# Optimization experiments

Hardware: AMD Instinct MI355X
Metric: run time of the kernel (lower is better)

## Reference

```python
import jax, jax.numpy as jnp
import numpy as np

D_MODEL = 1024
NUM_HEADS = 16
D_K = D_MODEL // NUM_HEADS
SCALE = D_K ** -0.5
NEG = -1e9


def _split_heads(t):
    B, L, D = t.shape
    return t.reshape(B, L, NUM_HEADS, D_K).transpose(0, 2, 1, 3)  # (B,H,L,dk)


def _tropical_scores(Q, K):
    # max over d_k of Q[...,i,d] + K[...,j,d] without materializing (B,H,L,L,dk)
    Qd = jnp.moveaxis(Q, -1, 0)  # (dk,B,H,L)
    Kd = jnp.moveaxis(K, -1, 0)
    B, H, L, _ = Q.shape
    init = jnp.full((B, H, L, L), -jnp.inf, Q.dtype)
    def step(carry, qk):
        q, k = qk  # (B,H,L) each
        return jnp.maximum(carry, q[..., :, None] + k[..., None, :]), None
    out, _ = jax.lax.scan(step, init, (Qd, Kd))
    return out


def setup_inputs() -> dict:
    key = jax.random.key(0)
    ks = jax.random.split(key, 10)
    B, L = 2, 1024
    x = jax.random.normal(ks[0], (B, L, D_MODEL), dtype=jnp.float32)
    # causal mask (B,1,L,L)
    mask = jnp.broadcast_to(jnp.tril(jnp.ones((L, L), dtype=bool)), (B, 1, L, L))
    s = 0.02
    Wq = jax.random.normal(ks[1], (D_MODEL, D_MODEL), jnp.float32) * s
    Wk = jax.random.normal(ks[2], (D_MODEL, D_MODEL), jnp.float32) * s
    Wv = jax.random.normal(ks[3], (D_MODEL, D_MODEL), jnp.float32) * s
    Wo = jax.random.normal(ks[4], (D_MODEL, D_MODEL), jnp.float32) * s
    bq = jnp.zeros((D_MODEL,), jnp.float32)
    bk = jnp.zeros((D_MODEL,), jnp.float32)
    bv = jnp.zeros((D_MODEL,), jnp.float32)
    bo = jnp.zeros((D_MODEL,), jnp.float32)
    # score_gate: weight zero-init, bias = -2.0 (as in torch module)
    Wg = jnp.zeros((NUM_HEADS, D_MODEL), jnp.float32)
    bg = jnp.full((NUM_HEADS,), -2.0, jnp.float32)
    # log temperatures, init_temp=1.0 -> log(1)=0
    log_temps = jnp.zeros((NUM_HEADS,), jnp.float32)
    return {"x": x, "mask": mask, "Wq": Wq, "bq": bq, "Wk": Wk, "bk": bk,
            "Wv": Wv, "bv": bv, "Wo": Wo, "bo": bo, "Wg": Wg, "bg": bg,
            "log_temps": log_temps}


def reference(x, mask, Wq, bq, Wk, bk, Wv, bv, Wo, bo, Wg, bg, log_temps):
    B, L, D = x.shape
    Q = _split_heads(x @ Wq.T + bq)
    K = _split_heads(x @ Wk.T + bk)
    V = _split_heads(x @ Wv.T + bv)
    class_scores = jnp.einsum('bhqd,bhkd->bhqk', Q, K) * SCALE
    trop_scores = _tropical_scores(Q, K) * SCALE
    # per-query, per-head gate g in (0,1): (B,L,H) -> (B,H,L,1)
    g = jax.nn.sigmoid(x @ Wg.T + bg).transpose(0, 2, 1)[..., None]
    scores = g * trop_scores + (1.0 - g) * class_scores
    scores = jnp.where(mask, scores, NEG)
    tau = jnp.clip(jnp.exp(log_temps), 0.02, 10.0).reshape(1, NUM_HEADS, 1, 1)
    attn = jax.nn.softmax(scores / tau, axis=-1)
    out = jnp.einsum('bhqk,bhkd->bhqd', attn, V)
    out = out.transpose(0, 2, 1, 3).reshape(B, L, D)
    return out @ Wo.T + bo, attn
```

## Files before the change

kernel.cpp:

```cpp
#include <hip/hip_runtime.h>


typedef _Float16 f16;
typedef __attribute__((ext_vector_type(2))) _Float16 h2;
typedef __attribute__((ext_vector_type(8))) _Float16 f16x8;
typedef __attribute__((ext_vector_type(4))) float f32x4;

__device__ inline f32x4 mfma_f16(f16x8 a, f16x8 b, f32x4 c) {
    return __builtin_amdgcn_mfma_f32_16x16x32_f16(a, b, c, 0, 0, 0);
}

__device__ inline void async_copy16(const f16* g, f16* l) {
    __builtin_amdgcn_global_load_lds((const __attribute__((address_space(1))) void*)g,
                                     (__attribute__((address_space(3))) void*)l, 16, 0, 0);
}

__device__ inline float dot2acc(h2 a, h2 b, float c) {
#if __has_builtin(__builtin_amdgcn_fdot2)
    return __builtin_amdgcn_fdot2(a, b, c, false);
#else
    c = fmaf((float)a[0], (float)b[0], c);
    return fmaf((float)a[1], (float)b[1], c);
#endif
}

__global__ __launch_bounds__(256) void cvt_all(const float* __restrict__ x,
                                               const float* __restrict__ Wq,
                                               const float* __restrict__ Wk,
                                               const float* __restrict__ Wv,
                                               const float* __restrict__ Wo,
                                               const float* __restrict__ Wg,
                                               f16* __restrict__ x16,
                                               f16* __restrict__ w16,
                                               f16* __restrict__ wo16) {
    int i = blockIdx.x * 256 + threadIdx.x;
    if (i >= 1576960) {
        int off = i - 1576960;
        *(uint2*)(w16 + (size_t)(3088 << 10) + (size_t)off * 4) = make_uint2(0u, 0u);
        return;
    }
    const float* s;
    f16* d;
    int off;
    if (i < 524288)       { s = x;  d = x16;                        off = i; }
    else if (i < 786432)  { s = Wq; d = w16;                        off = i - 524288; }
    else if (i < 1048576) { s = Wk; d = w16 + (1 << 20);            off = i - 786432; }
    else if (i < 1310720) { s = Wv; d = w16 + (2 << 20);            off = i - 1048576; }
    else if (i < 1572864) { s = Wo; d = wo16;                       off = i - 1310720; }
    else                  { s = Wg; d = w16 + (size_t)(3072 << 10); off = i - 1572864; }
    float4 v = *(const float4*)(s + (size_t)off * 4);
    f16 o[4] = {(f16)v.x, (f16)v.y, (f16)v.z, (f16)v.w};
    *(uint2*)(d + (size_t)off * 4) = *(uint2*)o;
}

template <bool OUT16, bool VTR, bool GATE>
__global__ __launch_bounds__(256) void gemm128(const f16* __restrict__ A,
                                               const f16* __restrict__ B,
                                               void* __restrict__ Cv,
                                               const float* __restrict__ b0,
                                               const float* __restrict__ b1,
                                               const float* __restrict__ b2,
                                               const float* __restrict__ bgv,
                                               f16* __restrict__ vt,
                                               float* __restrict__ gbuf,
                                               int K, int lda, int ldb, int ldc) {
    __shared__ f16 At[128 * 32];
    __shared__ f16 Bt[64 * 32];
    const int t = threadIdx.x;
    const int m0 = blockIdx.y * 128, n0 = blockIdx.x * 64;
    const int wave = t >> 6, lane = t & 63;
    const int l16 = lane & 15, quad = lane >> 4;
    const int wm = (wave >> 1) * 64, wn = (wave & 1) * 32;
    const int sr = t >> 2, sc = (t & 3) * 8;
    f32x4 acc[4][2] = {};
    for (int k0 = 0; k0 < K; k0 += 32) {
        __syncthreads();
#pragma unroll
        for (int i = 0; i < 2; ++i)
            async_copy16(A + (size_t)(m0 + sr + i * 64) * lda + k0 + sc, &At[t * 8 + i * 2048]);
        async_copy16(B + (size_t)(n0 + sr) * ldb + k0 + sc, &Bt[t * 8]);
        __syncthreads();
        f16x8 af[4], bfr[2];
#pragma unroll
        for (int i = 0; i < 4; ++i)
            af[i] = *(const f16x8*)&At[(wm + i * 16 + l16) * 32 + quad * 8];
#pragma unroll
        for (int i = 0; i < 2; ++i)
            bfr[i] = *(const f16x8*)&Bt[(wn + i * 16 + l16) * 32 + quad * 8];
#pragma unroll
        for (int mi = 0; mi < 4; ++mi)
#pragma unroll
            for (int ni = 0; ni < 2; ++ni)
                acc[mi][ni] = mfma_f16(af[mi], bfr[ni], acc[mi][ni]);
    }
#pragma unroll
    for (int mi = 0; mi < 4; ++mi) {
#pragma unroll
        for (int ni = 0; ni < 2; ++ni) {
            int gcol = n0 + wn + ni * 16 + l16;
            if (GATE && n0 >= 3072) {
                int hd = gcol - 3072;
                if (hd < 16) {
                    float bias = bgv[hd];
#pragma unroll
                    for (int rg = 0; rg < 4; ++rg) {
                        int grow = m0 + wm + mi * 16 + quad * 4 + rg;
                        float v = acc[mi][ni][rg] + bias;
                        gbuf[(size_t)grow * 16 + hd] = 1.0f / (1.0f + __expf(-v));
                    }
                }
            } else if (VTR && n0 >= 2048) {
                const float* bp = b2;
                float bias = bp[gcol & 1023];
                int hd = gcol - 2048;
                int h = hd >> 6, d = hd & 63;
                int k0r = m0 + wm + mi * 16 + quad * 4;
                int b = k0r >> 10;
                f16 o4[4];
#pragma unroll
                for (int rg = 0; rg < 4; ++rg) o4[rg] = (f16)(acc[mi][ni][rg] + bias);
                *(uint2*)&vt[((size_t)((b * 16 + h) * 64 + d)) * 1024 + (k0r & 1023)] =
                    *(uint2*)o4;
            } else {
                const float* bp = (gcol < 1024) ? b0 : (gcol < 2048 ? b1 : b2);
                float bias = bp[gcol & 1023];
#pragma unroll
                for (int rg = 0; rg < 4; ++rg) {
                    int grow = m0 + wm + mi * 16 + quad * 4 + rg;
                    float v = acc[mi][ni][rg] + bias;
                    if (OUT16)
                        ((f16*)Cv)[(size_t)grow * ldc + gcol] = (f16)v;
                    else
                        ((float*)Cv)[(size_t)grow * ldc + gcol] = v;
                }
            }
        }
    }
}

__global__ __launch_bounds__(256) void scores_fused(const f16* __restrict__ qkv16,
                                                    const f16* __restrict__ vt16,
                                                    const float* __restrict__ gbuf,
                                                    const float* __restrict__ log_temps,
                                                    float* __restrict__ attn,
                                                    f16* __restrict__ oh) {
    __shared__ f16 Qs[16][64];
    __shared__ f16 Ssm[16][1032];
    __shared__ float gsm[16];
    const int t = threadIdx.x;
    const int qt = 63 - (blockIdx.x >> 5);
    const int bh = blockIdx.x & 31;
    const int b = bh & 1, h = bh >> 1;
    const int q0 = qt << 4;
    {
        int rr = t >> 4, cc = (t & 15) * 4;
        *(uint2*)&Qs[rr][cc] =
            *(const uint2*)(qkv16 + (size_t)(b * 1024 + q0 + rr) * 3072 + h * 64 + cc);
    }
    if (t < 16) gsm[t] = gbuf[(size_t)(b * 1024 + q0 + t) * 16 + h];
    float tau = __expf(log_temps[h]);
    tau = fminf(fmaxf(tau, 0.02f), 10.0f);
    const float invtau = 1.0f / tau;
    __syncthreads();

    const int qmax = q0 + 15;
    const int npass = (qmax >> 9) + 1;
    for (int p = 0; p < npass; ++p) {
        const int k1 = (p << 9) + t;
        const int k2 = k1 + 256;
        const bool a1 = (k1 <= qmax), a2 = (k2 <= qmax);
        if (a1) {
            const f16* Kp1 = qkv16 + (size_t)(b * 1024 + k1) * 3072 + 1024 + h * 64;
            h2 kr1[32], kr2[32];
#pragma unroll
            for (int i = 0; i < 8; ++i) *(f16x8*)&kr1[i * 4] = ((const f16x8*)Kp1)[i];
            if (a2) {
                const f16* Kp2 = qkv16 + (size_t)(b * 1024 + k2) * 3072 + 1024 + h * 64;
#pragma unroll
                for (int i = 0; i < 8; ++i) *(f16x8*)&kr2[i * 4] = ((const f16x8*)Kp2)[i];
            }
#pragma unroll 2
            for (int q = 0; q < 16; ++q) {
                h2 qr[32];
#pragma unroll
                for (int i = 0; i < 8; ++i) *(f16x8*)&qr[i * 4] = *(const f16x8*)&Qs[q][i * 8];
                float g = gsm[q];
                {
                    float dot = 0.f;
                    h2 tm2 = {(f16)-65504.f, (f16)-65504.f};
#pragma unroll
                    for (int i = 0; i < 32; ++i) {
                        h2 qa = qr[i];
                        h2 s2 = qa + kr1[i];
                        tm2 = __builtin_elementwise_max(tm2, s2);
                        dot = dot2acc(qa, kr1[i], dot);
                    }
                    float tm = fmaxf((float)tm2[0], (float)tm2[1]);
                    Ssm[q][k1] = (f16)((g * tm + (1.0f - g) * dot) * 0.125f);
                }
                if (a2) {
                    float dot = 0.f;
                    h2 tm2 = {(f16)-65504.f, (f16)-65504.f};
#pragma unroll
                    for (int i = 0; i < 32; ++i) {
                        h2 qa = qr[i];
                        h2 s2 = qa + kr2[i];
                        tm2 = __builtin_elementwise_max(tm2, s2);
                        dot = dot2acc(qa, kr2[i], dot);
                    }
                    float tm = fmaxf((float)tm2[0], (float)tm2[1]);
                    Ssm[q][k2] = (f16)((g * tm + (1.0f - g) * dot) * 0.125f);
                }
            }
        }
    }
    __syncthreads();

    const int lane = t & 63, w = t >> 6;
    const int l16 = lane & 15, quad = lane >> 4;
#pragma unroll
    for (int j = 0; j < 4; ++j) {
        int q = w * 4 + j;
        int qg = q0 + q;
        float m = -1e30f;
        for (int k = lane; k <= qg; k += 64) m = fmaxf(m, (float)Ssm[q][k]);
#pragma unroll
        for (int o = 32; o > 0; o >>= 1) m = fmaxf(m, __shfl_xor(m, o));
        float ssum = 0.f;
        for (int k = lane; k <= qg; k += 64) {
            float e = __expf(((float)Ssm[q][k] - m) * invtau);
            Ssm[q][k] = (f16)e;
            ssum += e;
        }
#pragma unroll
        for (int o = 32; o > 0; o >>= 1) ssum += __shfl_xor(ssum, o);
        float inv = 1.0f / ssum;
        float* orow = attn + ((size_t)((b * 16 + h) * 1024 + qg) << 10);
        for (int k = lane; k < 1024; k += 64) {
            float val = (k <= qg) ? (float)Ssm[q][k] * inv : 0.0f;
            orow[k] = val;
            Ssm[q][k] = (f16)val;
        }
    }
    __syncthreads();

    {
        const int dw = w * 16;
        f32x4 acc = {};
        const int nkt = (q0 + 47) >> 5;
        const f16* Vb = vt16 + ((size_t)((b * 16 + h) * 64 + dw + l16)) * 1024 + quad * 8;
#pragma unroll 4
        for (int kt = 0; kt < nkt; ++kt) {
            const int kb = kt << 5;
            f16x8 a = *(const f16x8*)&Ssm[l16][kb + quad * 8];
            f16x8 bf = *(const f16x8*)(Vb + kb);
            acc = mfma_f16(a, bf, acc);
        }
#pragma unroll
        for (int rg = 0; rg < 4; ++rg)
            oh[(size_t)(b * 1024 + q0 + quad * 4 + rg) * 1024 + h * 64 + dw + l16] =
                (f16)acc[rg];
    }
}

extern "C" void kernel_launch(void* const* d_in, const int* in_sizes, int n_in,
                              void* d_out, int out_size, void* d_ws, size_t ws_size,
                              hipStream_t stream) {
    const float* x  = (const float*)d_in[0];
    const float* Wq = (const float*)d_in[2];
    const float* bq = (const float*)d_in[3];
    const float* Wk = (const float*)d_in[4];
    const float* bk = (const float*)d_in[5];
    const float* Wv = (const float*)d_in[6];
    const float* bv = (const float*)d_in[7];
    const float* Wo = (const float*)d_in[8];
    const float* bo = (const float*)d_in[9];
    const float* Wg = (const float*)d_in[10];
    const float* bg = (const float*)d_in[11];
    const float* lt = (const float*)d_in[12];
    float* out = (float*)d_out;
    float* attn = out + (size_t)2 * 1024 * 1024;

    char* ws = (char*)d_ws;
    const size_t KB = (size_t)1 << 10;
    f16*   x16   = (f16*)ws;
    f16*   w16   = (f16*)(ws + 4096 * KB);
    f16*   wo16  = (f16*)(ws + 10368 * KB);
    f16*   qkv16 = (f16*)(ws + 12416 * KB);
    f16*   vt16  = (f16*)(ws + 24704 * KB);
    float* gbuf  = (float*)(ws + 28800 * KB);
    f16*   oh16  = (f16*)(ws + 28928 * KB);

    cvt_all<<<6208, 256, 0, stream>>>(x, Wq, Wk, Wv, Wo, Wg, x16, w16, wo16);
    gemm128<true, true, true><<<dim3(49, 16), 256, 0, stream>>>(
        x16, w16, qkv16, bq, bk, bv, bg, vt16, gbuf, 1024, 1024, 1024, 3072);
    scores_fused<<<2048, 256, 0, stream>>>(qkv16, vt16, gbuf, lt, attn, oh16);
    gemm128<false, false, false><<<dim3(16, 16), 256, 0, stream>>>(
        oh16, wo16, out, bo, bo, bo, nullptr, nullptr, nullptr, 1024, 1024, 1024, 1024);
}
```

Measured before the change: 298.9 us.

## Use 64x64 GEMM for output projection and pair adjacent keys in scores kernel

Three changes in one edit. The output projection now uses a new 64x64-tile MFMA GEMM launched on a 16x32 grid, replacing the 128-tile GEMM that used only 256 blocks and so left many compute units idle. In the scores kernel each thread now handles two adjacent keys instead of keys 256 apart, which removes the second bounds check and merges the two f16 score stores into one 32-bit LDS store. The scores kernel also gets a waves-per-EU hint of 4 to raise occupancy, which may force register spilling given its large per-thread register arrays.

```diff
diff --git a/kernel.cpp b/kernel.cpp
--- a/kernel.cpp
+++ b/kernel.cpp
@@ -138,12 +138,59 @@
     }
 }
 
-__global__ __launch_bounds__(256) void scores_fused(const f16* __restrict__ qkv16,
-                                                    const f16* __restrict__ vt16,
-                                                    const float* __restrict__ gbuf,
-                                                    const float* __restrict__ log_temps,
-                                                    float* __restrict__ attn,
-                                                    f16* __restrict__ oh) {
+__global__ __launch_bounds__(256) void gemm64(const f16* __restrict__ A,
+                                              const f16* __restrict__ B,
+                                              float* __restrict__ C,
+                                              const float* __restrict__ b0,
+                                              int K, int lda, int ldb, int ldc) {
+    __shared__ f16 At[64 * 32];
+    __shared__ f16 Bt[64 * 32];
+    const int t = threadIdx.x;
+    const int m0 = blockIdx.y * 64, n0 = blockIdx.x * 64;
+    const int wave = t >> 6, lane = t & 63;
+    const int l16 = lane & 15, quad = lane >> 4;
+    const int wm = (wave >> 1) * 32, wn = (wave & 1) * 32;
+    const int sr = t >> 2, sc = (t & 3) * 8;
+    f32x4 acc[2][2] = {};
+    for (int k0 = 0; k0 < K; k0 += 32) {
+        __syncthreads();
+        async_copy16(A + (size_t)(m0 + sr) * lda + k0 + sc, &At[t * 8]);
+        async_copy16(B + (size_t)(n0 + sr) * ldb + k0 + sc, &Bt[t * 8]);
+        __syncthreads();
+        f16x8 af[2], bf[2];
+#pragma unroll
+        for (int i = 0; i < 2; ++i) {
+            af[i] = *(const f16x8*)&At[(wm + i * 16 + l16) * 32 + quad * 8];
+            bf[i] = *(const f16x8*)&Bt[(wn + i * 16 + l16) * 32 + quad * 8];
+        }
+#pragma unroll
+        for (int mi = 0; mi < 2; ++mi)
+#pragma unroll
+            for (int ni = 0; ni < 2; ++ni)
+                acc[mi][ni] = mfma_f16(af[mi], bf[ni], acc[mi][ni]);
+    }
+#pragma unroll
+    for (int mi = 0; mi < 2; ++mi) {
+#pragma unroll
+        for (int ni = 0; ni < 2; ++ni) {
+            int gcol = n0 + wn + ni * 16 + l16;
+            float bias = b0[gcol];
+#pragma unroll
+            for (int rg = 0; rg < 4; ++rg) {
+                int grow = m0 + wm + mi * 16 + quad * 4 + rg;
+                C[(size_t)grow * ldc + gcol] = acc[mi][ni][rg] + bias;
+            }
+        }
+    }
+}
+
+__global__ __launch_bounds__(256) __attribute__((amdgpu_waves_per_eu(4)))
+void scores_fused(const f16* __restrict__ qkv16,
+                  const f16* __restrict__ vt16,
+                  const float* __restrict__ gbuf,
+                  const float* __restrict__ log_temps,
+                  float* __restrict__ attn,
+                  f16* __restrict__ oh) {
     __shared__ f16 Qs[16][64];
     __shared__ f16 Ssm[16][1032];
     __shared__ float gsm[16];
@@ -166,18 +213,14 @@
     const int qmax = q0 + 15;
     const int npass = (qmax >> 9) + 1;
     for (int p = 0; p < npass; ++p) {
-        const int k1 = (p << 9) + t;
-        const int k2 = k1 + 256;
-        const bool a1 = (k1 <= qmax), a2 = (k2 <= qmax);
-        if (a1) {
+        const int k1 = (p << 9) + t * 2;
+        if (k1 <= qmax) {
             const f16* Kp1 = qkv16 + (size_t)(b * 1024 + k1) * 3072 + 1024 + h * 64;
             h2 kr1[32], kr2[32];
 #pragma unroll
-            for (int i = 0; i < 8; ++i) *(f16x8*)&kr1[i * 4] = ((const f16x8*)Kp1)[i];
-            if (a2) {
-                const f16* Kp2 = qkv16 + (size_t)(b * 1024 + k2) * 3072 + 1024 + h * 64;
-#pragma unroll
-                for (int i = 0; i < 8; ++i) *(f16x8*)&kr2[i * 4] = ((const f16x8*)Kp2)[i];
+            for (int i = 0; i < 8; ++i) {
+                *(f16x8*)&kr1[i * 4] = ((const f16x8*)Kp1)[i];
+                *(f16x8*)&kr2[i * 4] = *(const f16x8*)(Kp1 + 3072 + i * 8);
             }
 #pragma unroll 2
             for (int q = 0; q < 16; ++q) {
@@ -185,6 +228,7 @@
 #pragma unroll
                 for (int i = 0; i < 8; ++i) *(f16x8*)&qr[i * 4] = *(const f16x8*)&Qs[q][i * 8];
                 float g = gsm[q];
+                f16 o2[2];
                 {
                     float dot = 0.f;
                     h2 tm2 = {(f16)-65504.f, (f16)-65504.f};
@@ -196,9 +240,9 @@
                         dot = dot2acc(qa, kr1[i], dot);
                     }
                     float tm = fmaxf((float)tm2[0], (float)tm2[1]);
-                    Ssm[q][k1] = (f16)((g * tm + (1.0f - g) * dot) * 0.125f);
+                    o2[0] = (f16)((g * tm + (1.0f - g) * dot) * 0.125f);
                 }
-                if (a2) {
+                {
                     float dot = 0.f;
                     h2 tm2 = {(f16)-65504.f, (f16)-65504.f};
 #pragma unroll
@@ -209,8 +253,9 @@
                         dot = dot2acc(qa, kr2[i], dot);
                     }
                     float tm = fmaxf((float)tm2[0], (float)tm2[1]);
-                    Ssm[q][k2] = (f16)((g * tm + (1.0f - g) * dot) * 0.125f);
+                    o2[1] = (f16)((g * tm + (1.0f - g) * dot) * 0.125f);
                 }
+                *(unsigned int*)&Ssm[q][k1] = *(unsigned int*)o2;
             }
         }
     }
@@ -295,6 +340,5 @@
     gemm128<true, true, true><<<dim3(49, 16), 256, 0, stream>>>(
         x16, w16, qkv16, bq, bk, bv, bg, vt16, gbuf, 1024, 1024, 1024, 3072);
     scores_fused<<<2048, 256, 0, stream>>>(qkv16, vt16, gbuf, lt, attn, oh16);
-    gemm128<false, false, false><<<dim3(16, 16), 256, 0, stream>>>(
-        oh16, wo16, out, bo, bo, bo, nullptr, nullptr, nullptr, 1024, 1024, 1024, 1024);
-}
+    gemm64<<<dim3(16, 32), 256, 0, stream>>>(oh16, wo16, out, bo, 1024, 1024, 1024, 1024);
+}
```

New measurement: 317.2 us. +6.1%, slower.
